# Kernel optimization log

Hardware: AMD Instinct MI355X
Metric: run time of the kernel (lower is better)

The kernel has to match this reference:

```python
import jax, jax.numpy as jnp
import numpy as np

N = 65536      # tokens
H = 8          # num_heads
D = 64         # head_dim
G = 64         # num_slices
HID = H * D    # 512
EPS = 1e-5
SCALE = float(1.0 / np.sqrt(D))


def _lin(k, out_dim, in_dim):
    return (jax.random.normal(k, (out_dim, in_dim), jnp.float32) / np.sqrt(in_dim)).astype(jnp.float32)


def setup_inputs() -> dict:
    key = jax.random.key(0)
    ks = jax.random.split(key, 12)
    return {
        "x": jax.random.normal(ks[0], (N, HID), jnp.float32),
        "W_x": _lin(ks[1], HID, HID), "b_x": jnp.zeros((HID,), jnp.float32),
        "W_slice": _lin(ks[2], G, D), "b_slice": jnp.zeros((G,), jnp.float32),
        "W_t1": _lin(ks[3], G, D), "b_t1": jnp.zeros((G,), jnp.float32),
        "W_t2": _lin(ks[4], 1, G), "b_t2": jnp.zeros((1,), jnp.float32),
        "t_bias": jnp.ones((H, 1, 1), jnp.float32) * 0.5,
        "Wq": _lin(ks[5], D, D), "Wk": _lin(ks[6], D, D),
        "Wv": _lin(ks[7], D, D), "Wo": _lin(ks[8], D, D),
        "W_out": _lin(ks[9], HID, HID), "b_out": jnp.zeros((HID,), jnp.float32),
    }


def reference(x, W_x, b_x, W_slice, b_slice, W_t1, b_t1, W_t2, b_t2,
              t_bias, Wq, Wk, Wv, Wo, W_out, b_out):
    # project and split heads: [N,HID] -> [H,N,D]
    xp = x @ W_x.T + b_x
    x_mid = jnp.transpose(xp.reshape(-1, H, D), (1, 0, 2))

    # per-token temperature MLP: Linear(D,G) -> gelu -> Linear(G,1) -> gelu, + bias
    t = jax.nn.gelu(jax.nn.gelu(x_mid @ W_t1.T + b_t1) @ W_t2.T + b_t2) + t_bias
    t = jnp.clip(t, 0.01)  # [H,N,1]

    # slice logits + gumbel softmax routing weights [H,N,G]
    logits = x_mid @ W_slice.T + b_slice
    u = jax.random.uniform(jax.random.key(1), logits.shape, jnp.float32)
    gnoise = -jnp.log(-jnp.log(u + 1e-8) + 1e-8)
    w = jax.nn.softmax((logits + gnoise) / t, axis=-1)

    # weighted pooling into G slice tokens per head: [H,G,D]
    norm = w.sum(axis=1)  # [H,G]
    tokens = jnp.einsum('hnd,hng->hgd', x_mid, w) / (norm[..., None] + EPS)

    # tiny single-head self-attention over G slice tokens (shared weights, vmapped over H)
    q = tokens @ Wq.T
    k = tokens @ Wk.T
    v = tokens @ Wv.T
    attn = jax.nn.softmax(jnp.einsum('hgd,hGd->hgG', q * SCALE, k), axis=-1)
    o = jnp.einsum('hgG,hGd->hgd', attn, v) @ Wo.T  # [H,G,D]

    # weighted scatter-back to tokens, merge heads, output projection
    out = jnp.einsum('hgd,hng->hnd', o, w)
    out = jnp.transpose(out, (1, 0, 2)).reshape(-1, HID)
    return out @ W_out.T + b_out
```

## Files before the change

### kernel.cpp

```cpp
#include <hip/hip_runtime.h>
#include <stdint.h>

typedef unsigned short u16;
typedef __bf16 bf16x8 __attribute__((ext_vector_type(8)));
typedef float f32x4 __attribute__((ext_vector_type(4)));


__device__ __forceinline__ u16 f2bf(float f) {
  uint32_t u = __float_as_uint(f);
  uint32_t r = u + 0x7fffu + ((u >> 16) & 1u);
  return (u16)(r >> 16);
}
__device__ __forceinline__ float bf2f(u16 h) {
  return __uint_as_float(((uint32_t)h) << 16);
}

union BF8 { bf16x8 v; u16 u[8]; uint4 q4; };

__device__ __forceinline__ float gelu_fast(float x) {
  const float c = 0.79788456080286535588f;
  float z = c * fmaf(0.044715f, x * x * x, x);
  return x / (1.0f + __expf(-2.0f * z));
}

__device__ __forceinline__ uint32_t rotl32(uint32_t v, int s) {
  return (v << s) | (v >> (32 - s));
}

__device__ __forceinline__ uint32_t threefry_bits(uint32_t idx) {
  const uint32_t k0 = 0u, k1 = 1u;
  const uint32_t k2 = 0x1BD11BDAu ^ k0 ^ k1;
  uint32_t x0 = 0u + k0;
  uint32_t x1 = idx + k1;
#define TF_R(r) { x0 += x1; x1 = rotl32(x1, r); x1 ^= x0; }
  TF_R(13) TF_R(15) TF_R(26) TF_R(6)
  x0 += k1; x1 += k2 + 1u;
  TF_R(17) TF_R(29) TF_R(16) TF_R(24)
  x0 += k2; x1 += k0 + 2u;
  TF_R(13) TF_R(15) TF_R(26) TF_R(6)
  x0 += k0; x1 += k1 + 3u;
  TF_R(17) TF_R(29) TF_R(16) TF_R(24)
  x0 += k1; x1 += k2 + 4u;
  TF_R(13) TF_R(15) TF_R(26) TF_R(6)
  x0 += k2; x1 += k0 + 5u;
#undef TF_R
  return x0 ^ x1;
}

__device__ __forceinline__ void gload_lds16(const void* g, void* l) {
  __builtin_amdgcn_global_load_lds(
      (const __attribute__((address_space(1))) void*)g,
      (__attribute__((address_space(3))) void*)l, 16, 0, 0);
}

__global__ __launch_bounds__(256) void conv_split(
    const float* __restrict__ in, u16* __restrict__ hi, u16* __restrict__ lo,
    int nq)
{
  for (int i = blockIdx.x * 256 + threadIdx.x; i < nq; i += gridDim.x * 256) {
    float4 v = ((const float4*)in)[i];
    ushort4 h, l;
    h.x = f2bf(v.x); l.x = f2bf(v.x - bf2f(h.x));
    h.y = f2bf(v.y); l.y = f2bf(v.y - bf2f(h.y));
    h.z = f2bf(v.z); l.z = f2bf(v.z - bf2f(h.z));
    h.w = f2bf(v.w); l.w = f2bf(v.w - bf2f(h.w));
    ((ushort4*)hi)[i] = h;
    ((ushort4*)lo)[i] = l;
  }
}

__global__ __launch_bounds__(256) void gemm_split(
    const u16* __restrict__ Ah, const u16* __restrict__ Al,
    const u16* __restrict__ Bh, const u16* __restrict__ Bl,
    const float* __restrict__ bias, uint32_t* __restrict__ Cp)
{
  __shared__ u16 lds[4][4096];
  const int tid = threadIdx.x;
  const int lane = tid & 63;
  const int w = tid >> 6;
  const int vid = (blockIdx.x & 7) * 256 + (blockIdx.x >> 3);
  const int bn = vid & 3;
  const int bm = vid >> 2;
  const int wr = w >> 1, wc = w & 1;

  f32x4 acc[4][4];
#pragma unroll
  for (int m = 0; m < 4; ++m)
#pragma unroll
    for (int n = 0; n < 4; ++n) acc[m][n] = (f32x4){0.f, 0.f, 0.f, 0.f};

  const int srow = lane >> 2;
  const int scol = (lane & 3) * 8;

  for (int kt = 0; kt < 16; ++kt) {
    const int k0 = kt * 32;
    __syncthreads();
#pragma unroll
    for (int i = 0; i < 8; ++i) {
      const int mat = i & 3;
      const int rb = w * 2 + (i >> 2);
      const int row = rb * 16 + srow;
      const u16* base = (mat == 0) ? Ah : (mat == 1) ? Al
                       : (mat == 2) ? Bh : Bl;
      const int tbase = (mat < 2) ? bm * 128 : bn * 128;
      const u16* src = base + (size_t)(tbase + row) * 512 + k0 + scol;
      gload_lds16(src, &lds[mat][rb * 512]);
    }
    __syncthreads();

    bf16x8 ah[4], al[4], bh_[4], bl_[4];
    const int co = (lane >> 4) * 8;
    const int rr = lane & 15;
#pragma unroll
    for (int f = 0; f < 4; ++f) {
      const int ra  = (wr * 64 + f * 16 + rr) * 32 + co;
      const int rb2 = (wc * 64 + f * 16 + rr) * 32 + co;
      ah[f]  = *(const bf16x8*)&lds[0][ra];
      al[f]  = *(const bf16x8*)&lds[1][ra];
      bh_[f] = *(const bf16x8*)&lds[2][rb2];
      bl_[f] = *(const bf16x8*)&lds[3][rb2];
    }
#pragma unroll
    for (int m = 0; m < 4; ++m)
#pragma unroll
      for (int n = 0; n < 4; ++n) {
        acc[m][n] = __builtin_amdgcn_mfma_f32_16x16x32_bf16(ah[m], bh_[n], acc[m][n], 0, 0, 0);
        acc[m][n] = __builtin_amdgcn_mfma_f32_16x16x32_bf16(ah[m], bl_[n], acc[m][n], 0, 0, 0);
        acc[m][n] = __builtin_amdgcn_mfma_f32_16x16x32_bf16(al[m], bh_[n], acc[m][n], 0, 0, 0);
      }
  }

  const int cn0 = lane & 15;
  const int rm0 = (lane >> 4) * 4;
#pragma unroll
  for (int n = 0; n < 4; ++n) {
    const int ng = bn * 128 + wc * 64 + n * 16 + cn0;
    const float bv = bias[ng];
#pragma unroll
    for (int m = 0; m < 4; ++m) {
      const int mg = bm * 128 + wr * 64 + m * 16 + rm0;
#pragma unroll
      for (int r = 0; r < 4; ++r) {
        const float v = acc[m][n][r] + bv;
        const u16 hb = f2bf(v);
        const u16 lb = f2bf(v - bf2f(hb));
        Cp[(size_t)(mg + r) * 512 + ng] = (uint32_t)hb | ((uint32_t)lb << 16);
      }
    }
  }
}

__global__ __launch_bounds__(256) void gemm_packA(
    const uint32_t* __restrict__ A, const u16* __restrict__ Bh,
    const u16* __restrict__ Bl, const float* __restrict__ bias,
    float* __restrict__ C)
{
  __shared__ uint32_t ldsA[128 * 32];
  __shared__ u16 ldsBh[128 * 32], ldsBl[128 * 32];
  const int tid = threadIdx.x;
  const int lane = tid & 63;
  const int w = tid >> 6;
  const int vid = (blockIdx.x & 7) * 256 + (blockIdx.x >> 3);
  const int bn = vid & 3;
  const int bm = vid >> 2;
  const int wr = w >> 1, wcq = w & 1;

  f32x4 acc[4][4];
#pragma unroll
  for (int m = 0; m < 4; ++m)
#pragma unroll
    for (int n = 0; n < 4; ++n) acc[m][n] = (f32x4){0.f, 0.f, 0.f, 0.f};

  for (int kt = 0; kt < 16; ++kt) {
    const int k0 = kt * 32;
    __syncthreads();
#pragma unroll
    for (int i = 0; i < 4; ++i) {
      const int rb8 = i * 4 + w;
      const int row = rb8 * 8 + (lane >> 3);
      const uint32_t* src =
          A + (size_t)(bm * 128 + row) * 512 + k0 + (lane & 7) * 4;
      gload_lds16(src, &ldsA[rb8 * 8 * 32]);
    }
#pragma unroll
    for (int i = 0; i < 2; ++i) {
      const int rb16 = i * 4 + w;
      const int row = rb16 * 16 + (lane >> 2);
      const int sc = (lane & 3) * 8;
      gload_lds16(Bh + (size_t)(bn * 128 + row) * 512 + k0 + sc,
                  &ldsBh[rb16 * 16 * 32]);
      gload_lds16(Bl + (size_t)(bn * 128 + row) * 512 + k0 + sc,
                  &ldsBl[rb16 * 16 * 32]);
    }
    __syncthreads();

    bf16x8 ah[4], al[4], bh_[4], bl_[4];
    const int co = (lane >> 4) * 8;
    const int rr = lane & 15;
#pragma unroll
    for (int f = 0; f < 4; ++f) {
      const int ra = (wr * 64 + f * 16 + rr) * 32 + co;
      const uint4 p0 = *(const uint4*)&ldsA[ra];
      const uint4 p1 = *(const uint4*)&ldsA[ra + 4];
      BF8 hv, lv;
      uint32_t* hd = (uint32_t*)&hv.q4;
      uint32_t* ld = (uint32_t*)&lv.q4;
      hd[0] = __builtin_amdgcn_perm(p0.y, p0.x, 0x05040100u);
      hd[1] = __builtin_amdgcn_perm(p0.w, p0.z, 0x05040100u);
      hd[2] = __builtin_amdgcn_perm(p1.y, p1.x, 0x05040100u);
      hd[3] = __builtin_amdgcn_perm(p1.w, p1.z, 0x05040100u);
      ld[0] = __builtin_amdgcn_perm(p0.y, p0.x, 0x07060302u);
      ld[1] = __builtin_amdgcn_perm(p0.w, p0.z, 0x07060302u);
      ld[2] = __builtin_amdgcn_perm(p1.y, p1.x, 0x07060302u);
      ld[3] = __builtin_amdgcn_perm(p1.w, p1.z, 0x07060302u);
      ah[f] = hv.v; al[f] = lv.v;
      const int rb2 = (wcq * 64 + f * 16 + rr) * 32 + co;
      bh_[f] = *(const bf16x8*)&ldsBh[rb2];
      bl_[f] = *(const bf16x8*)&ldsBl[rb2];
    }
#pragma unroll
    for (int m = 0; m < 4; ++m)
#pragma unroll
      for (int n = 0; n < 4; ++n) {
        acc[m][n] = __builtin_amdgcn_mfma_f32_16x16x32_bf16(ah[m], bh_[n], acc[m][n], 0, 0, 0);
        acc[m][n] = __builtin_amdgcn_mfma_f32_16x16x32_bf16(ah[m], bl_[n], acc[m][n], 0, 0, 0);
        acc[m][n] = __builtin_amdgcn_mfma_f32_16x16x32_bf16(al[m], bh_[n], acc[m][n], 0, 0, 0);
      }
  }

  const int cn0 = lane & 15;
  const int rm0 = (lane >> 4) * 4;
#pragma unroll
  for (int n = 0; n < 4; ++n) {
    const int ng = bn * 128 + wcq * 64 + n * 16 + cn0;
    const float bv = bias[ng];
#pragma unroll
    for (int m = 0; m < 4; ++m) {
      const int mg = bm * 128 + wr * 64 + m * 16 + rm0;
#pragma unroll
      for (int r = 0; r < 4; ++r)
        C[(size_t)(mg + r) * 512 + ng] = acc[m][n][r] + bv;
    }
  }
}

__global__ __launch_bounds__(256, 4) void k2_route(
    const uint32_t* __restrict__ xpq, const float* __restrict__ Wsl,
    const float* __restrict__ bsl, const float* __restrict__ Wt1,
    const float* __restrict__ bt1, const float* __restrict__ Wt2,
    const float* __restrict__ bt2, const float* __restrict__ tbias,
    uint32_t* __restrict__ wcp)
{
  __shared__ u16 Wf[2][8][2][64][8];
  __shared__ uint32_t wbuf[4][16][68];

  const int tid = threadIdx.x;
  const int l = tid & 63, wid = tid >> 6;
  const int l15 = l & 15, q = l >> 4;
  const int h = blockIdx.x >> 8;
  const int chunk = blockIdx.x & 255;

#pragma unroll
  for (int it = 0; it < 8; ++it) {
    const int slot = tid + it * 256;
    const int p = slot >> 10;
    const int rest = slot & 1023;
    const int nn = rest >> 7;
    const int kk = (rest >> 6) & 1;
    const int sl = rest & 63;
    const int row = nn * 16 + (sl & 15);
    const int kb = kk * 32 + (sl >> 4) * 8;
    const float* src = (row < 64) ? (Wsl + row * 64 + kb)
                                  : (Wt1 + (row - 64) * 64 + kb);
#pragma unroll
    for (int e = 0; e < 8; ++e) {
      const float v = src[e];
      const u16 hb = f2bf(v);
      Wf[p][nn][kk][sl][e] = (p == 0) ? hb : f2bf(v - bf2f(hb));
    }
  }
  __syncthreads();

  float bslv[4], bt1v[4], wt2v[4];
#pragma unroll
  for (int j = 0; j < 4; ++j) {
    bslv[j] = bsl[j * 16 + l15];
    bt1v[j] = bt1[j * 16 + l15];
    wt2v[j] = Wt2[j * 16 + l15];
  }
  const float bt2v = bt2[0], tbv = tbias[h];

#pragma unroll 1
  for (int tm = 0; tm < 4; ++tm) {
    const int n0t = chunk * 256 + (tm >> 1) * 128 + wid * 32 + (tm & 1) * 16;

    bf16x8 ah[2], al[2];
#pragma unroll
    for (int kk = 0; kk < 2; ++kk) {
      const uint32_t* sp = xpq + (size_t)(n0t + l15) * 512 + h * 64
                           + kk * 32 + q * 8;
      const uint4 p0 = *(const uint4*)sp;
      const uint4 p1 = *(const uint4*)(sp + 4);
      BF8 hv, lv;
      uint32_t* hd = (uint32_t*)&hv.q4;
      uint32_t* ld = (uint32_t*)&lv.q4;
      hd[0] = __builtin_amdgcn_perm(p0.y, p0.x, 0x05040100u);
      hd[1] = __builtin_amdgcn_perm(p0.w, p0.z, 0x05040100u);
      hd[2] = __builtin_amdgcn_perm(p1.y, p1.x, 0x05040100u);
      hd[3] = __builtin_amdgcn_perm(p1.w, p1.z, 0x05040100u);
      ld[0] = __builtin_amdgcn_perm(p0.y, p0.x, 0x07060302u);
      ld[1] = __builtin_amdgcn_perm(p0.w, p0.z, 0x07060302u);
      ld[2] = __builtin_amdgcn_perm(p1.y, p1.x, 0x07060302u);
      ld[3] = __builtin_amdgcn_perm(p1.w, p1.z, 0x07060302u);
      ah[kk] = hv.v; al[kk] = lv.v;
    }

    f32x4 acc[8];
#pragma unroll
    for (int n = 0; n < 8; ++n) acc[n] = (f32x4){0.f, 0.f, 0.f, 0.f};
#pragma unroll
    for (int kk = 0; kk < 2; ++kk)
#pragma unroll
      for (int nn = 0; nn < 8; ++nn) {
        BF8 whf, wlf;
        whf.q4 = *(const uint4*)&Wf[0][nn][kk][l][0];
        wlf.q4 = *(const uint4*)&Wf[1][nn][kk][l][0];
        acc[nn] = __builtin_amdgcn_mfma_f32_16x16x32_bf16(ah[kk], whf.v, acc[nn], 0, 0, 0);
        acc[nn] = __builtin_amdgcn_mfma_f32_16x16x32_bf16(ah[kk], wlf.v, acc[nn], 0, 0, 0);
        acc[nn] = __builtin_amdgcn_mfma_f32_16x16x32_bf16(al[kk], whf.v, acc[nn], 0, 0, 0);
      }

    float itv[4];
#pragma unroll
    for (int r = 0; r < 4; ++r) {
      float part = 0.f;
#pragma unroll
      for (int j = 0; j < 4; ++j)
        part += gelu_fast(acc[4 + j][r] + bt1v[j]) * wt2v[j];
      part += __shfl_xor(part, 1);
      part += __shfl_xor(part, 2);
      part += __shfl_xor(part, 4);
      part += __shfl_xor(part, 8);
      const float tval = gelu_fast(part + bt2v) + tbv;
      itv[r] = 1.0f / fmaxf(tval, 0.01f);
    }

    const uint32_t pbase = ((uint32_t)((h << 16) | (n0t + q * 4))) << 6;
#pragma unroll
    for (int j = 0; j < 4; ++j) {
      const uint32_t cc = j * 16 + l15;
#pragma unroll
      for (int r = 0; r < 4; ++r) {
        const uint32_t bits = threefry_bits(pbase + ((uint32_t)r << 6) + cc);
        const float u = __uint_as_float((bits >> 9) | 0x3f800000u) - 1.0f;
        const float gin = -__logf(u + 1e-8f);
        const float gn = -__logf(gin + 1e-8f);
        acc[j][r] = (acc[j][r] + bslv[j] + gn) * itv[r];
      }
    }

#pragma unroll
    for (int r = 0; r < 4; ++r) {
      float mx = fmaxf(fmaxf(acc[0][r], acc[1][r]),
                       fmaxf(acc[2][r], acc[3][r]));
      mx = fmaxf(mx, __shfl_xor(mx, 1));
      mx = fmaxf(mx, __shfl_xor(mx, 2));
      mx = fmaxf(mx, __shfl_xor(mx, 4));
      mx = fmaxf(mx, __shfl_xor(mx, 8));
      float se = 0.f;
#pragma unroll
      for (int j = 0; j < 4; ++j) {
        const float e = __expf(acc[j][r] - mx);
        acc[j][r] = e;
        se += e;
      }
      se += __shfl_xor(se, 1);
      se += __shfl_xor(se, 2);
      se += __shfl_xor(se, 4);
      se += __shfl_xor(se, 8);
      const float inv = 1.0f / se;
#pragma unroll
      for (int j = 0; j < 4; ++j) acc[j][r] *= inv;
    }

#pragma unroll
    for (int j = 0; j < 4; ++j)
#pragma unroll
      for (int r = 0; r < 4; ++r) {
        const float wv = acc[j][r];
        const u16 hb = f2bf(wv);
        const u16 lb = f2bf(wv - bf2f(hb));
        wbuf[wid][q * 4 + r][j * 16 + l15] = (uint32_t)hb | ((uint32_t)lb << 16);
      }
    __syncthreads();

#pragma unroll
    for (int it = 0; it < 4; ++it) {
      const int t = l >> 2;
      const int qq = (l & 3) + it * 4;
      const uint4 v = *(const uint4*)&wbuf[wid][t][qq * 4];
      *(uint4*)(wcp + (size_t)(n0t + t) * 512 + h * 64 + qq * 4) = v;
    }
    __syncthreads();
  }
}

__global__ __launch_bounds__(256, 2) void k3_pool(
    const uint32_t* __restrict__ xpq, const uint32_t* __restrict__ wcp,
    float* __restrict__ tok_num, float* __restrict__ nrm)
{
  __shared__ float red[64][65];
  const int h = blockIdx.x >> 6;
  const int chunk = blockIdx.x & 63;
  const int lane = threadIdx.x & 63;
  const int wid = threadIdx.x >> 6;
  const int l15 = lane & 15, q = lane >> 4;

  f32x4 acc[4][4];
#pragma unroll
  for (int m = 0; m < 4; ++m)
#pragma unroll
    for (int n = 0; n < 4; ++n) acc[m][n] = (f32x4){0.f, 0.f, 0.f, 0.f};
  float csum[4] = {0.f, 0.f, 0.f, 0.f};

  const int tw = chunk * 1024 + wid * 256;
#pragma unroll 1
  for (int tt = 0; tt < 8; ++tt) {
    const int t0 = tw + tt * 32;
    uint32_t wreg[4][8], xreg[4][8];
#pragma unroll
    for (int e = 0; e < 8; ++e) {
      const size_t rb = (size_t)(t0 + q * 8 + e) * 512 + h * 64 + l15;
#pragma unroll
      for (int m = 0; m < 4; ++m) {
        wreg[m][e] = wcp[rb + m * 16];
        xreg[m][e] = xpq[rb + m * 16];
      }
    }
    bf16x8 whf[4], wlf[4], xhf[4], xlf[4];
#pragma unroll
    for (int m = 0; m < 4; ++m) {
      BF8 hv, lv, xh, xl;
      uint32_t* hd = (uint32_t*)&hv.q4;
      uint32_t* ld = (uint32_t*)&lv.q4;
      uint32_t* xhd = (uint32_t*)&xh.q4;
      uint32_t* xld = (uint32_t*)&xl.q4;
#pragma unroll
      for (int p = 0; p < 4; ++p) {
        hd[p]  = __builtin_amdgcn_perm(wreg[m][2*p+1], wreg[m][2*p], 0x05040100u);
        ld[p]  = __builtin_amdgcn_perm(wreg[m][2*p+1], wreg[m][2*p], 0x07060302u);
        xhd[p] = __builtin_amdgcn_perm(xreg[m][2*p+1], xreg[m][2*p], 0x05040100u);
        xld[p] = __builtin_amdgcn_perm(xreg[m][2*p+1], xreg[m][2*p], 0x07060302u);
      }
      whf[m] = hv.v; wlf[m] = lv.v; xhf[m] = xh.v; xlf[m] = xl.v;
#pragma unroll
      for (int e = 0; e < 8; ++e)
        csum[m] += __uint_as_float(wreg[m][e] << 16)
                 + __uint_as_float(wreg[m][e] & 0xffff0000u);
    }
#pragma unroll
    for (int m = 0; m < 4; ++m)
#pragma unroll
      for (int n = 0; n < 4; ++n) {
        acc[m][n] = __builtin_amdgcn_mfma_f32_16x16x32_bf16(whf[m], xhf[n], acc[m][n], 0, 0, 0);
        acc[m][n] = __builtin_amdgcn_mfma_f32_16x16x32_bf16(whf[m], xlf[n], acc[m][n], 0, 0, 0);
        acc[m][n] = __builtin_amdgcn_mfma_f32_16x16x32_bf16(wlf[m], xhf[n], acc[m][n], 0, 0, 0);
      }
  }

#pragma unroll
  for (int m = 0; m < 4; ++m) {
    csum[m] += __shfl_xor(csum[m], 16);
    csum[m] += __shfl_xor(csum[m], 32);
  }
  if (q == 0) {
#pragma unroll
    for (int m = 0; m < 4; ++m)
      atomicAdd(&nrm[h * 64 + m * 16 + l15], csum[m]);
  }

  for (int w = 0; w < 4; ++w) {
    if (wid == w) {
#pragma unroll
      for (int m = 0; m < 4; ++m)
#pragma unroll
        for (int n = 0; n < 4; ++n)
#pragma unroll
          for (int r = 0; r < 4; ++r) {
            const int g = m * 16 + q * 4 + r;
            const int d = n * 16 + l15;
            if (w == 0) red[g][d] = acc[m][n][r];
            else        red[g][d] += acc[m][n][r];
          }
    }
    __syncthreads();
  }
  for (int e = threadIdx.x; e < 4096; e += 256)
    atomicAdd(&tok_num[h * 4096 + e], red[e >> 6][e & 63]);
}

__global__ __launch_bounds__(256) void k4_attn(
    const float* __restrict__ tok_num, const float* __restrict__ nrm,
    const float* __restrict__ Wq, const float* __restrict__ Wk,
    const float* __restrict__ Wv, const float* __restrict__ Wo,
    float* __restrict__ o_out)
{
  __shared__ float T[64][65], Abuf[64][65], Bbuf[64][65], Wbuf[64][65], S2[64][65];
  const int h = blockIdx.x;
  const int tid = threadIdx.x;

  for (int e = tid; e < 4096; e += 256) {
    const int g = e >> 6, d = e & 63;
    T[g][d] = tok_num[h * 4096 + e] / (nrm[h * 64 + g] + 1e-5f);
  }
  for (int e = tid; e < 4096; e += 256) Wbuf[e >> 6][e & 63] = Wq[e];
  __syncthreads();

  const int g = tid >> 2, d0 = (tid & 3) * 16;
  float r[16];

#pragma unroll
  for (int j = 0; j < 16; ++j) r[j] = 0.f;
  for (int e = 0; e < 64; ++e) {
    const float tv = T[g][e];
#pragma unroll
    for (int j = 0; j < 16; ++j) r[j] = fmaf(tv, Wbuf[d0 + j][e], r[j]);
  }
#pragma unroll
  for (int j = 0; j < 16; ++j) Abuf[g][d0 + j] = r[j];
  __syncthreads();

  for (int e = tid; e < 4096; e += 256) Wbuf[e >> 6][e & 63] = Wk[e];
  __syncthreads();

#pragma unroll
  for (int j = 0; j < 16; ++j) r[j] = 0.f;
  for (int e = 0; e < 64; ++e) {
    const float tv = T[g][e];
#pragma unroll
    for (int j = 0; j < 16; ++j) r[j] = fmaf(tv, Wbuf[d0 + j][e], r[j]);
  }
#pragma unroll
  for (int j = 0; j < 16; ++j) Bbuf[g][d0 + j] = r[j];
  __syncthreads();

#pragma unroll
  for (int j = 0; j < 16; ++j) r[j] = 0.f;
  for (int e = 0; e < 64; ++e) {
    const float qv = Abuf[g][e] * 0.125f;
#pragma unroll
    for (int j = 0; j < 16; ++j) r[j] = fmaf(qv, Bbuf[d0 + j][e], r[j]);
  }
#pragma unroll
  for (int j = 0; j < 16; ++j) S2[g][d0 + j] = r[j];
  __syncthreads();

  if (tid < 64) {
    float mx = -1e30f;
    for (int j = 0; j < 64; ++j) mx = fmaxf(mx, S2[tid][j]);
    float sum = 0.f;
    for (int j = 0; j < 64; ++j) {
      const float e2 = expf(S2[tid][j] - mx);
      S2[tid][j] = e2;
      sum += e2;
    }
    const float inv = 1.0f / sum;
    for (int j = 0; j < 64; ++j) S2[tid][j] *= inv;
  }
  __syncthreads();

  for (int e = tid; e < 4096; e += 256) Wbuf[e >> 6][e & 63] = Wv[e];
  __syncthreads();

#pragma unroll
  for (int j = 0; j < 16; ++j) r[j] = 0.f;
  for (int e = 0; e < 64; ++e) {
    const float tv = T[g][e];
#pragma unroll
    for (int j = 0; j < 16; ++j) r[j] = fmaf(tv, Wbuf[d0 + j][e], r[j]);
  }
  __syncthreads();
#pragma unroll
  for (int j = 0; j < 16; ++j) Bbuf[g][d0 + j] = r[j];
  __syncthreads();

#pragma unroll
  for (int j = 0; j < 16; ++j) r[j] = 0.f;
  for (int e = 0; e < 64; ++e) {
    const float sv = S2[g][e];
#pragma unroll
    for (int j = 0; j < 16; ++j) r[j] = fmaf(sv, Bbuf[e][d0 + j], r[j]);
  }
  __syncthreads();
#pragma unroll
  for (int j = 0; j < 16; ++j) Abuf[g][d0 + j] = r[j];
  for (int e = tid; e < 4096; e += 256) Wbuf[e >> 6][e & 63] = Wo[e];
  __syncthreads();

#pragma unroll
  for (int j = 0; j < 16; ++j) r[j] = 0.f;
  for (int e = 0; e < 64; ++e) {
    const float ov = Abuf[g][e];
#pragma unroll
    for (int j = 0; j < 16; ++j) r[j] = fmaf(ov, Wbuf[d0 + j][e], r[j]);
  }
#pragma unroll
  for (int j = 0; j < 16; ++j) o_out[h * 4096 + g * 64 + d0 + j] = r[j];
}

__global__ __launch_bounds__(256) void k4b_m2(
    const float* __restrict__ o, const float* __restrict__ Wout,
    u16* __restrict__ M2h, u16* __restrict__ M2l)
{
  const int j = blockIdx.x >> 1;
  const int hg = ((blockIdx.x & 1) << 8) + threadIdx.x;
  const int h = hg >> 6;
  const float* orow = &o[hg * 64];
  const float* wrow = &Wout[j * 512 + h * 64];
  float s = 0.f;
#pragma unroll
  for (int d = 0; d < 64; ++d) s = fmaf(orow[d], wrow[d], s);
  const u16 hb = f2bf(s);
  M2h[j * 512 + hg] = hb;
  M2l[j * 512 + hg] = f2bf(s - bf2f(hb));
}

extern "C" void kernel_launch(void* const* d_in, const int* in_sizes, int n_in,
                              void* d_out, int out_size, void* d_ws, size_t ws_size,
                              hipStream_t stream)
{
  const float* x      = (const float*)d_in[0];
  const float* W_x    = (const float*)d_in[1];
  const float* b_x    = (const float*)d_in[2];
  const float* W_sl   = (const float*)d_in[3];
  const float* b_sl   = (const float*)d_in[4];
  const float* W_t1   = (const float*)d_in[5];
  const float* b_t1   = (const float*)d_in[6];
  const float* W_t2   = (const float*)d_in[7];
  const float* b_t2   = (const float*)d_in[8];
  const float* t_bias = (const float*)d_in[9];
  const float* Wq     = (const float*)d_in[10];
  const float* Wk     = (const float*)d_in[11];
  const float* Wv     = (const float*)d_in[12];
  const float* Wo     = (const float*)d_in[13];
  const float* W_out  = (const float*)d_in[14];
  const float* b_out  = (const float*)d_in[15];

  float* out = (float*)d_out;
  uint32_t* xpq = (uint32_t*)d_out;

  char* ws = (char*)d_ws;
  u16*      Ahi   = (u16*)(ws);
  u16*      Alo   = (u16*)(ws + 67108864);
  uint32_t* wcp   = (uint32_t*)(ws);
  u16*      Bhi   = (u16*)(ws + 134217728);
  u16*      Blo   = (u16*)(ws + 134742016);
  float* tok_num  = (float*)(ws + 135266304);
  float* nrm      = (float*)(ws + 135397376);
  float* o_buf    = (float*)(ws + 135399424);

  conv_split<<<2048, 256, 0, stream>>>(x, Ahi, Alo, 8388608);
  conv_split<<<256, 256, 0, stream>>>(W_x, Bhi, Blo, 65536);
  gemm_split<<<2048, 256, 0, stream>>>(Ahi, Alo, Bhi, Blo, b_x, xpq);

  hipMemsetAsync(tok_num, 0, 133120, stream);

  k2_route<<<2048, 256, 0, stream>>>(xpq, W_sl, b_sl, W_t1, b_t1, W_t2, b_t2,
                                     t_bias, wcp);
  k3_pool<<<512, 256, 0, stream>>>(xpq, wcp, tok_num, nrm);
  k4_attn<<<8, 256, 0, stream>>>(tok_num, nrm, Wq, Wk, Wv, Wo, o_buf);
  k4b_m2<<<1024, 256, 0, stream>>>(o_buf, W_out, Bhi, Blo);
  gemm_packA<<<2048, 256, 0, stream>>>(wcp, Bhi, Blo, b_out, out);
}
```

Baseline: 554.9 us.

## Fuse fp32-to-bf16 split of x into the first GEMM's A-operand load

Removes the conv_split pass over x (128MB read, 128MB hi/lo written) by having the GEMM read fp32 rows of x directly into registers and split them into bf16 hi/lo fragments in-kernel, staging only the B operand through LDS. It also drops two __syncthreads in the routing kernel's write-back, relying on each wave touching only its own wbuf slice. In exchange the GEMM issues direct global fp32 loads that are not shared across waves (each A row is reread by the two column waves) and spends extra ALU on conversion inside the k-loop.

Result: slower. 607.4 us (+9.5%).

```diff
diff --git a/kernel.cpp b/kernel.cpp
--- a/kernel.cpp
+++ b/kernel.cpp
@@ -69,12 +69,12 @@
   }
 }
 
-__global__ __launch_bounds__(256) void gemm_split(
-    const u16* __restrict__ Ah, const u16* __restrict__ Al,
-    const u16* __restrict__ Bh, const u16* __restrict__ Bl,
-    const float* __restrict__ bias, uint32_t* __restrict__ Cp)
-{
-  __shared__ u16 lds[4][4096];
+__global__ __launch_bounds__(256) void gemm_fA(
+    const float* __restrict__ A, const u16* __restrict__ Bh,
+    const u16* __restrict__ Bl, const float* __restrict__ bias,
+    uint32_t* __restrict__ Cp)
+{
+  __shared__ u16 ldsBh[128 * 32], ldsBl[128 * 32];
   const int tid = threadIdx.x;
   const int lane = tid & 63;
   const int w = tid >> 6;
@@ -89,36 +89,53 @@
 #pragma unroll
     for (int n = 0; n < 4; ++n) acc[m][n] = (f32x4){0.f, 0.f, 0.f, 0.f};
 
-  const int srow = lane >> 2;
-  const int scol = (lane & 3) * 8;
+  const int co = (lane >> 4) * 8;
+  const int rr = lane & 15;
 
   for (int kt = 0; kt < 16; ++kt) {
     const int k0 = kt * 32;
     __syncthreads();
 #pragma unroll
-    for (int i = 0; i < 8; ++i) {
-      const int mat = i & 3;
-      const int rb = w * 2 + (i >> 2);
-      const int row = rb * 16 + srow;
-      const u16* base = (mat == 0) ? Ah : (mat == 1) ? Al
-                       : (mat == 2) ? Bh : Bl;
-      const int tbase = (mat < 2) ? bm * 128 : bn * 128;
-      const u16* src = base + (size_t)(tbase + row) * 512 + k0 + scol;
-      gload_lds16(src, &lds[mat][rb * 512]);
+    for (int i = 0; i < 4; ++i) {
+      const int plane = i >> 1;
+      const int rb16 = (i & 1) * 4 + w;
+      const int row = rb16 * 16 + (lane >> 2);
+      const int sc = (lane & 3) * 8;
+      const u16* src = ((plane == 0) ? Bh : Bl)
+                       + (size_t)(bn * 128 + row) * 512 + k0 + sc;
+      gload_lds16(src, (plane == 0) ? &ldsBh[rb16 * 16 * 32]
+                                    : &ldsBl[rb16 * 16 * 32]);
+    }
+    float4 a0[4], a1[4];
+#pragma unroll
+    for (int f = 0; f < 4; ++f) {
+      const float* ap = A + (size_t)(bm * 128 + wr * 64 + f * 16 + rr) * 512
+                        + k0 + co;
+      a0[f] = *(const float4*)ap;
+      a1[f] = *(const float4*)(ap + 4);
+    }
+    bf16x8 ah[4], al[4];
+#pragma unroll
+    for (int f = 0; f < 4; ++f) {
+      const float vv[8] = {a0[f].x, a0[f].y, a0[f].z, a0[f].w,
+                           a1[f].x, a1[f].y, a1[f].z, a1[f].w};
+      BF8 hv, lv;
+#pragma unroll
+      for (int e = 0; e < 8; ++e) {
+        const u16 hb = f2bf(vv[e]);
+        hv.u[e] = hb;
+        lv.u[e] = f2bf(vv[e] - bf2f(hb));
+      }
+      ah[f] = hv.v; al[f] = lv.v;
     }
     __syncthreads();
 
-    bf16x8 ah[4], al[4], bh_[4], bl_[4];
-    const int co = (lane >> 4) * 8;
-    const int rr = lane & 15;
+    bf16x8 bh_[4], bl_[4];
 #pragma unroll
     for (int f = 0; f < 4; ++f) {
-      const int ra  = (wr * 64 + f * 16 + rr) * 32 + co;
       const int rb2 = (wc * 64 + f * 16 + rr) * 32 + co;
-      ah[f]  = *(const bf16x8*)&lds[0][ra];
-      al[f]  = *(const bf16x8*)&lds[1][ra];
-      bh_[f] = *(const bf16x8*)&lds[2][rb2];
-      bl_[f] = *(const bf16x8*)&lds[3][rb2];
+      bh_[f] = *(const bf16x8*)&ldsBh[rb2];
+      bl_[f] = *(const bf16x8*)&ldsBl[rb2];
     }
 #pragma unroll
     for (int m = 0; m < 4; ++m)
@@ -392,7 +409,6 @@
         const u16 lb = f2bf(wv - bf2f(hb));
         wbuf[wid][q * 4 + r][j * 16 + l15] = (uint32_t)hb | ((uint32_t)lb << 16);
       }
-    __syncthreads();
 
 #pragma unroll
     for (int it = 0; it < 4; ++it) {
@@ -401,7 +417,6 @@
       const uint4 v = *(const uint4*)&wbuf[wid][t][qq * 4];
       *(uint4*)(wcp + (size_t)(n0t + t) * 512 + h * 64 + qq * 4) = v;
     }
-    __syncthreads();
   }
 }
 
@@ -650,8 +665,6 @@
   uint32_t* xpq = (uint32_t*)d_out;
 
   char* ws = (char*)d_ws;
-  u16*      Ahi   = (u16*)(ws);
-  u16*      Alo   = (u16*)(ws + 67108864);
   uint32_t* wcp   = (uint32_t*)(ws);
   u16*      Bhi   = (u16*)(ws + 134217728);
   u16*      Blo   = (u16*)(ws + 134742016);
@@ -659,9 +672,8 @@
   float* nrm      = (float*)(ws + 135397376);
   float* o_buf    = (float*)(ws + 135399424);
 
-  conv_split<<<2048, 256, 0, stream>>>(x, Ahi, Alo, 8388608);
   conv_split<<<256, 256, 0, stream>>>(W_x, Bhi, Blo, 65536);
-  gemm_split<<<2048, 256, 0, stream>>>(Ahi, Alo, Bhi, Blo, b_x, xpq);
+  gemm_fA<<<2048, 256, 0, stream>>>(x, Bhi, Blo, b_x, xpq);
 
   hipMemsetAsync(tok_num, 0, 133120, stream);
 
```
